# Kernel tuning notes

Measured on AMD Instinct MI355X. Metric: run time of the kernel, lower is better.

## Reference

```python
import jax, jax.numpy as jnp
import numpy as np

D_MODEL = 768
NUM_HEADS = 12
D_K = D_MODEL // NUM_HEADS


def setup_inputs() -> dict:
    key = jax.random.key(0)
    ks = jax.random.split(key, 11)
    B, S, D = 2, 4096, D_MODEL
    s = 1.0 / np.sqrt(D)
    return {
        "query": jax.random.normal(ks[0], (B, S, D), jnp.float32),
        "key": jax.random.normal(ks[1], (B, S, D), jnp.float32),
        "value": jax.random.normal(ks[2], (B, S, D), jnp.float32),
        "Wq": jax.random.normal(ks[3], (D, D), jnp.float32) * s,
        "bq": jnp.zeros((D,), jnp.float32),
        "Wk": jax.random.normal(ks[4], (D, D), jnp.float32) * s,
        "bk": jnp.zeros((D,), jnp.float32),
        "Wv": jax.random.normal(ks[5], (D, D), jnp.float32) * s,
        "bv": jnp.zeros((D,), jnp.float32),
        "Wo": jax.random.normal(ks[6], (D, D), jnp.float32) * s,
        "bo": jnp.zeros((D,), jnp.float32),
    }


def reference(query, key, value, Wq, bq, Wk, bk, Wv, bv, Wo, bo):
    B, S, D = query.shape
    H, dk = NUM_HEADS, D_K
    # torch Linear: y = x @ W^T + b
    def proj(x, W, b):
        return (x @ W.T + b).reshape(B, S, H, dk).transpose(0, 2, 1, 3)  # [B,H,S,dk]
    q = proj(query, Wq, bq)
    k = proj(key, Wk, bk)
    v = proj(value, Wv, bv)
    scores = jnp.einsum("bhqd,bhkd->bhqk", q, k) / jnp.sqrt(jnp.float32(dk))
    attn = jax.nn.softmax(scores, axis=-1)  # dropout is identity in eval mode
    x = jnp.einsum("bhqk,bhkd->bhqd", attn, v)
    x = x.transpose(0, 2, 1, 3).reshape(B, S, D)
    return x @ Wo.T + bo
```

## Files before the change

### kernel.cpp

```cpp
#include <hip/hip_runtime.h>
#include <hip/hip_bf16.h>


typedef __attribute__((ext_vector_type(8))) short short8;
typedef __attribute__((ext_vector_type(4))) float floatx4;
typedef __attribute__((ext_vector_type(4))) float float4v;

#define S_LEN 4096
#define D_MODEL 768
#define NUM_HEADS 12
#define DK 64
#define BATCH 2
#define M_ROWS (BATCH * S_LEN)
#define HEADS_TOTAL (BATCH * NUM_HEADS)
#define QSCALE 0.1803368801111204f

__device__ __forceinline__ unsigned short f2bf(float f) {
    union { float f; unsigned int i; } v; v.f = f;
    unsigned int r = v.i + 0x7fff + ((v.i >> 16) & 1);
    return (unsigned short)(r >> 16);
}

__device__ __forceinline__ unsigned int cvt_pk_bf16(float a, float b) {
    unsigned int r;
    asm("v_cvt_pk_bf16_f32 %0, %1, %2" : "=v"(r) : "v"(a), "v"(b));
    return r;
}

__device__ __forceinline__ float exp2_fast(float x) {
    float r;
    asm("v_exp_f32 %0, %1" : "=v"(r) : "v"(x));
    return r;
}

__device__ __forceinline__ int swz(int r, int c) {
    return (r << 6) + ((((c >> 3) ^ (r & 7)) << 3) | (c & 7));
}

__device__ __forceinline__ void pack8(const float4v& f0, const float4v& f1,
                                      unsigned short* __restrict__ dst) {
    uint4 w;
    w.x = cvt_pk_bf16(f0[0], f0[1]);
    w.y = cvt_pk_bf16(f0[2], f0[3]);
    w.z = cvt_pk_bf16(f1[0], f1[1]);
    w.w = cvt_pk_bf16(f1[2], f1[3]);
    *(uint4*)dst = w;
}

__device__ __forceinline__ void bar_lgkm() {
    asm volatile("s_waitcnt lgkmcnt(0)" ::: "memory");
    __builtin_amdgcn_s_barrier();
    __builtin_amdgcn_sched_barrier(0);
}

template <int MODE, int XF32>
__global__ __launch_bounds__(256, 2) void gemm_bt(
    const void* __restrict__ Xv,
    const float* __restrict__ W,
    const float* __restrict__ bias,
    void* __restrict__ outv,
    int M, int N, int K)
{
    __shared__ __align__(16) unsigned short As[2][8192];
    __shared__ __align__(16) unsigned short Bs[2][6144];

    const int t    = threadIdx.x;
    const int wv   = t >> 6;
    const int lane = t & 63;
    const int l15  = lane & 15;
    const int quad = lane >> 4;
    const int wm   = wv >> 1;
    const int wn   = wv & 1;

    const int bid = blockIdx.x;
    const int wg  = (bid & 7) * 64 + (bid >> 3);
    const int m0  = (wg >> 3) * 128;
    const int n0  = (wg & 7) * 96;

    floatx4 acc[4][3];
#pragma unroll
    for (int i = 0; i < 4; ++i)
#pragma unroll
        for (int j = 0; j < 3; ++j) acc[i][j] = (floatx4){0.f, 0.f, 0.f, 0.f};

    const int sr   = t >> 3;
    const int scol = (t & 7) * 8;
    const int st0  = swz(sr, scol);

    float4v xaE[8], xaO[8];
    uint4   xuE[4], xuO[4];
    float4v waE[6], waO[6];

#define G_LOAD(xa, xu, wa, step)                                                         \
    do {                                                                                 \
        const long kofs = (long)(step) * 64 + scol;                                      \
        _Pragma("unroll")                                                                \
        for (int p = 0; p < 4; ++p) {                                                    \
            if (XF32) {                                                                  \
                const float* xp = (const float*)Xv + (long)(m0 + sr + 32 * p) * K + kofs; \
                xa[2 * p]     = *(const float4v*)xp;                                     \
                xa[2 * p + 1] = *(const float4v*)(xp + 4);                               \
            } else {                                                                     \
                const unsigned short* xp =                                               \
                    (const unsigned short*)Xv + (long)(m0 + sr + 32 * p) * K + kofs;     \
                xu[p] = *(const uint4*)xp;                                               \
            }                                                                            \
        }                                                                                \
        _Pragma("unroll")                                                                \
        for (int p = 0; p < 3; ++p) {                                                    \
            const float* wp = W + (long)(n0 + sr + 32 * p) * K + kofs;                   \
            wa[2 * p]     = *(const float4v*)wp;                                         \
            wa[2 * p + 1] = *(const float4v*)(wp + 4);                                   \
        }                                                                                \
    } while (0)

#define G_WRITE(xa, xu, wa, buf)                                                         \
    do {                                                                                 \
        _Pragma("unroll")                                                                \
        for (int p = 0; p < 4; ++p) {                                                    \
            if (XF32) pack8(xa[2 * p], xa[2 * p + 1], &As[buf][st0 + p * 2048]);         \
            else      *(uint4*)(&As[buf][st0 + p * 2048]) = xu[p];                       \
        }                                                                                \
        _Pragma("unroll")                                                                \
        for (int p = 0; p < 3; ++p)                                                      \
            pack8(wa[2 * p], wa[2 * p + 1], &Bs[buf][st0 + p * 2048]);                   \
    } while (0)

#define DO_MFMA(buf)                                                                     \
    do {                                                                                 \
        const unsigned short* Ab = &As[buf][0];                                          \
        const unsigned short* Bb = &Bs[buf][0];                                          \
        _Pragma("unroll")                                                                \
        for (int kk = 0; kk < 2; ++kk) {                                                 \
            short8 af[4];                                                                \
            _Pragma("unroll")                                                            \
            for (int mi = 0; mi < 4; ++mi)                                               \
                af[mi] = *(const short8*)(Ab + swz(wm * 64 + mi * 16 + l15, kk * 32 + quad * 8)); \
            _Pragma("unroll")                                                            \
            for (int nj = 0; nj < 3; ++nj) {                                             \
                short8 bf = *(const short8*)(Bb + swz(wn * 48 + nj * 16 + l15, kk * 32 + quad * 8)); \
                _Pragma("unroll")                                                        \
                for (int mi = 0; mi < 4; ++mi)                                           \
                    acc[mi][nj] = __builtin_amdgcn_mfma_f32_16x16x32_bf16(af[mi], bf, acc[mi][nj], 0, 0, 0); \
            }                                                                            \
        }                                                                                \
    } while (0)

    const int NS = K / 64;

    G_LOAD(xaE, xuE, waE, 0);
    G_WRITE(xaE, xuE, waE, 0);
    G_LOAD(xaO, xuO, waO, 1);
    __syncthreads();

    for (int s = 0; s < NS - 2; s += 2) {
        DO_MFMA(0);
        G_WRITE(xaO, xuO, waO, 1);
        G_LOAD(xaE, xuE, waE, s + 2);
        bar_lgkm();
        DO_MFMA(1);
        G_WRITE(xaE, xuE, waE, 0);
        if (s + 3 < NS) G_LOAD(xaO, xuO, waO, s + 3);
        bar_lgkm();
    }
    DO_MFMA(0);
    G_WRITE(xaO, xuO, waO, 1);
    bar_lgkm();
    DO_MFMA(1);

#undef G_LOAD
#undef G_WRITE
#undef DO_MFMA

    if (MODE == 2) {
        unsigned short* Sx = &As[0][0];
        __syncthreads();
#pragma unroll
        for (int nj = 0; nj < 3; ++nj) {
            const int colL = wn * 48 + nj * 16 + l15;
            const float bvv = bias[n0 + colL];
#pragma unroll
            for (int mi = 0; mi < 4; ++mi)
#pragma unroll
                for (int reg = 0; reg < 4; ++reg) {
                    const int row = wm * 64 + mi * 16 + quad * 4 + reg;
                    Sx[row * 97 + colL] = f2bf(acc[mi][nj][reg] + bvv);
                }
        }
        __syncthreads();
        const int bb2 = m0 >> 12;
        const int slb = m0 & 4095;
#pragma unroll
        for (int p = 0; p < 6; ++p) {
            const int ci   = t + (p << 8);
            const int colL = ci >> 4;
            const int s8   = (ci & 15) << 3;
            const int dg   = n0 + colL;
            const int h    = dg >> 6;
            const int d    = dg & 63;
            unsigned short w[8];
#pragma unroll
            for (int j = 0; j < 8; ++j) w[j] = Sx[(s8 + j) * 97 + colL];
            unsigned short* outp = (unsigned short*)outv +
                ((long)((bb2 * NUM_HEADS + h) * DK + d)) * S_LEN + slb + s8;
            *(uint4*)outp = *(uint4*)w;
        }
        return;
    }

#pragma unroll
    for (int nj = 0; nj < 3; ++nj) {
        const int col = n0 + wn * 48 + nj * 16 + l15;
        const float bv = bias[col];
#pragma unroll
        for (int mi = 0; mi < 4; ++mi)
#pragma unroll
            for (int reg = 0; reg < 4; ++reg) {
                const int row = m0 + wm * 64 + mi * 16 + quad * 4 + reg;
                const float o = acc[mi][nj][reg] + bv;
                if (MODE == 0) {
                    ((float*)outv)[(long)row * N + col] = o;
                } else {
                    const int bb = row >> 12;
                    const int ss = row & 4095;
                    const int h  = col >> 6;
                    const int d  = col & 63;
                    ((unsigned short*)outv)[(((long)bb * NUM_HEADS + h) * S_LEN + ss) * DK + d] = f2bf(o);
                }
            }
    }
}

__global__ __launch_bounds__(256, 6) void flash_attn_fused(
    const float* __restrict__ Xq,
    const float* __restrict__ Wq,
    const float* __restrict__ bq,
    const unsigned short* __restrict__ Kg,
    const unsigned short* __restrict__ VTg,
    unsigned short* __restrict__ ctx)
{
    __shared__ __align__(16) unsigned short Ks[4096];
    __shared__ __align__(16) unsigned short Vt[4096];
    __shared__ __align__(16) unsigned short Pq[4096];

    const int t    = threadIdx.x;
    const int wv   = t >> 6;
    const int lane = t & 63;
    const int l15  = lane & 15;
    const int quad = lane >> 4;
    const int q0   = blockIdx.x * 64;
    const int bh   = blockIdx.y;
    const int bb   = bh / NUM_HEADS;
    const int h    = bh % NUM_HEADS;
    const long kbase = (long)bh * S_LEN * DK;
    const long vbase = (long)bh * DK * S_LEN;

    const int srow = t >> 3;
    const int scol = (t & 7) * 8;

    const int st_a = swz(srow, scol);
    const int st_b = swz(32 + srow, scol);

    {
        floatx4 qacc[4];
#pragma unroll
        for (int i = 0; i < 4; ++i) qacc[i] = (floatx4){0.f, 0.f, 0.f, 0.f};

        for (int k0 = 0; k0 < D_MODEL; k0 += 64) {
            {
                const float* xp = Xq + ((long)bb * S_LEN + q0 + srow) * D_MODEL + k0 + scol;
                float4v a0 = *(const float4v*)xp, a1 = *(const float4v*)(xp + 4);
                const float* xp2 = xp + (long)32 * D_MODEL;
                float4v a2 = *(const float4v*)xp2, a3 = *(const float4v*)(xp2 + 4);
                const float* wp = Wq + (long)(h * DK + srow) * D_MODEL + k0 + scol;
                float4v b0 = *(const float4v*)wp, b1 = *(const float4v*)(wp + 4);
                const float* wp2 = wp + (long)32 * D_MODEL;
                float4v b2 = *(const float4v*)wp2, b3 = *(const float4v*)(wp2 + 4);
                pack8(a0, a1, &Ks[st_a]); pack8(a2, a3, &Ks[st_b]);
                pack8(b0, b1, &Vt[st_a]); pack8(b2, b3, &Vt[st_b]);
            }
            __syncthreads();
#pragma unroll
            for (int kk = 0; kk < 2; ++kk) {
                short8 a = *(const short8*)(&Ks[swz(wv * 16 + l15, kk * 32 + quad * 8)]);
#pragma unroll
                for (int nj = 0; nj < 4; ++nj) {
                    short8 b = *(const short8*)(&Vt[swz(nj * 16 + l15, kk * 32 + quad * 8)]);
                    qacc[nj] = __builtin_amdgcn_mfma_f32_16x16x32_bf16(a, b, qacc[nj], 0, 0, 0);
                }
            }
            __syncthreads();
        }
#pragma unroll
        for (int nj = 0; nj < 4; ++nj) {
            const float bv = bq[h * DK + nj * 16 + l15];
#pragma unroll
            for (int reg = 0; reg < 4; ++reg) {
                const int row = wv * 16 + quad * 4 + reg;
                Pq[swz(row, nj * 16 + l15)] = f2bf((qacc[nj][reg] + bv) * QSCALE);
            }
        }
    }

    uint4 kr0 = *(const uint4*)(Kg + kbase + (long)srow * DK + scol);
    uint4 kr1 = *(const uint4*)(Kg + kbase + (long)(32 + srow) * DK + scol);
    uint4 vr0 = *(const uint4*)(VTg + vbase + (long)srow * S_LEN + scol);
    uint4 vr1 = *(const uint4*)(VTg + vbase + (long)(32 + srow) * S_LEN + scol);

    asm volatile("s_waitcnt lgkmcnt(0)" ::: "memory");
    short8 qfrag[2];
#pragma unroll
    for (int kk = 0; kk < 2; ++kk)
        qfrag[kk] = *(const short8*)(&Pq[swz(wv * 16 + l15, kk * 32 + quad * 8)]);

    *(uint4*)(&Ks[st_a]) = kr0; *(uint4*)(&Ks[st_b]) = kr1;
    *(uint4*)(&Vt[st_a]) = vr0; *(uint4*)(&Vt[st_b]) = vr1;
    __syncthreads();

    float l_loc = 0.f;
    floatx4 acc[4];
#pragma unroll
    for (int i = 0; i < 4; ++i) acc[i] = (floatx4){0.f, 0.f, 0.f, 0.f};

    const unsigned short* kp = Kg + kbase + (long)64 * DK;
    const unsigned short* vp = VTg + vbase + 64;

    for (int tix = 0; tix < 64; ++tix) {
        if (tix < 63) {
            kr0 = *(const uint4*)(kp + (long)srow * DK + scol);
            kr1 = *(const uint4*)(kp + (long)(32 + srow) * DK + scol);
            vr0 = *(const uint4*)(vp + (long)srow * S_LEN + scol);
            vr1 = *(const uint4*)(vp + (long)(32 + srow) * S_LEN + scol);
            kp += (long)64 * DK;
            vp += 64;
        }

        floatx4 sc[4];
#pragma unroll
        for (int i = 0; i < 4; ++i) sc[i] = (floatx4){0.f, 0.f, 0.f, 0.f};
        __builtin_amdgcn_s_setprio(1);
#pragma unroll
        for (int kk = 0; kk < 2; ++kk) {
#pragma unroll
            for (int nj = 0; nj < 4; ++nj) {
                short8 kf = *(const short8*)(&Ks[swz(nj * 16 + l15, kk * 32 + quad * 8)]);
                sc[nj] = __builtin_amdgcn_mfma_f32_16x16x32_bf16(kf, qfrag[kk], sc[nj], 0, 0, 0);
            }
        }
        __builtin_amdgcn_s_setprio(0);

#pragma unroll
        for (int nj = 0; nj < 4; ++nj) {
            const float e0 = exp2_fast(sc[nj][0]);
            const float e1 = exp2_fast(sc[nj][1]);
            const float e2 = exp2_fast(sc[nj][2]);
            const float e3 = exp2_fast(sc[nj][3]);
            l_loc += (e0 + e1) + (e2 + e3);
            uint2 w;
            w.x = cvt_pk_bf16(e0, e1);
            w.y = cvt_pk_bf16(e2, e3);
            *(uint2*)(&Pq[swz(wv * 16 + l15, nj * 16 + quad * 4)]) = w;
        }
        asm volatile("s_waitcnt lgkmcnt(0)" ::: "memory");

        __builtin_amdgcn_s_setprio(1);
#pragma unroll
        for (int kk = 0; kk < 2; ++kk) {
            short8 a = *(const short8*)(&Pq[swz(wv * 16 + l15, kk * 32 + quad * 8)]);
#pragma unroll
            for (int dj = 0; dj < 4; ++dj) {
                short8 b = *(const short8*)(&Vt[swz(dj * 16 + l15, kk * 32 + quad * 8)]);
                acc[dj] = __builtin_amdgcn_mfma_f32_16x16x32_bf16(a, b, acc[dj], 0, 0, 0);
            }
        }
        __builtin_amdgcn_s_setprio(0);

        __syncthreads();
        if (tix < 63) {
            *(uint4*)(&Ks[st_a]) = kr0; *(uint4*)(&Ks[st_b]) = kr1;
            *(uint4*)(&Vt[st_a]) = vr0; *(uint4*)(&Vt[st_b]) = vr1;
        }
        __syncthreads();
    }

    float l_full = l_loc;
    l_full += __shfl_xor(l_full, 16);
    l_full += __shfl_xor(l_full, 32);
    float l_row[4];
#pragma unroll
    for (int reg = 0; reg < 4; ++reg)
        l_row[reg] = __shfl(l_full, quad * 4 + reg);
#pragma unroll
    for (int dj = 0; dj < 4; ++dj) {
#pragma unroll
        for (int reg = 0; reg < 4; ++reg) {
            const int ss = q0 + wv * 16 + quad * 4 + reg;
            const float v = acc[dj][reg] / l_row[reg];
            ctx[((long)bb * S_LEN + ss) * D_MODEL + h * DK + dj * 16 + l15] = f2bf(v);
        }
    }
}

__global__ void fill_sentinel(float* out, long n, float val) {
    long i = (long)blockIdx.x * blockDim.x + threadIdx.x;
    if (i < n) out[i] = val;
}

extern "C" void kernel_launch(void* const* d_in, const int* in_sizes, int n_in,
                              void* d_out, int out_size, void* d_ws, size_t ws_size,
                              hipStream_t stream)
{
    const float* q_in = (const float*)d_in[0];
    const float* k_in = (const float*)d_in[1];
    const float* v_in = (const float*)d_in[2];
    const float* Wq = (const float*)d_in[3];
    const float* bq = (const float*)d_in[4];
    const float* Wk = (const float*)d_in[5];
    const float* bk = (const float*)d_in[6];
    const float* Wv = (const float*)d_in[7];
    const float* bv = (const float*)d_in[8];
    const float* Wo = (const float*)d_in[9];
    const float* bo = (const float*)d_in[10];

    const long NELEM = (long)M_ROWS * D_MODEL;
    const size_t needed = (size_t)(3 * NELEM) * sizeof(unsigned short);

    if (ws_size < needed) {
        const long n = (long)out_size;
        fill_sentinel<<<(n + 255) / 256, 256, 0, stream>>>((float*)d_out, n,
                                                           (float)(ws_size >> 20));
        return;
    }

    unsigned short* ws  = (unsigned short*)d_ws;
    unsigned short* kp  = ws;
    unsigned short* vtp = ws + NELEM;
    unsigned short* ctx = ws + 2 * NELEM;

    const int GG = (M_ROWS / 128) * (D_MODEL / 96);
    gemm_bt<1, 1><<<GG, 256, 0, stream>>>(k_in, Wk, bk, kp, M_ROWS, D_MODEL, D_MODEL);
    gemm_bt<2, 1><<<GG, 256, 0, stream>>>(v_in, Wv, bv, vtp, M_ROWS, D_MODEL, D_MODEL);

    dim3 agrid(S_LEN / 64, HEADS_TOTAL);
    flash_attn_fused<<<agrid, 256, 0, stream>>>(q_in, Wq, bq, kp, vtp, ctx);

    gemm_bt<0, 0><<<GG, 256, 0, stream>>>(ctx, Wo, bo, d_out, M_ROWS, D_MODEL, D_MODEL);
}
```

Baseline: 381.2 us.

## Process two 64-row query groups per attention block to reuse K/V tiles

Each attention workgroup now handles 128 query rows (two groups of 64) instead of 64, so every K and V tile loaded into shared memory feeds twice the MFMA work. This halves global K/V traffic and per-tile barrier overhead relative to compute. In exchange it doubles accumulator and score registers, grows the P/Q shared buffer, lowers the launch-bounds occupancy hint from 6 to 3, and halves the grid size.

```diff
diff --git a/kernel.cpp b/kernel.cpp
--- a/kernel.cpp
+++ b/kernel.cpp
@@ -231,7 +231,7 @@
     }
 }
 
-__global__ __launch_bounds__(256, 6) void flash_attn_fused(
+__global__ __launch_bounds__(256, 3) void flash_attn_fused(
     const float* __restrict__ Xq,
     const float* __restrict__ Wq,
     const float* __restrict__ bq,
@@ -241,14 +241,14 @@
 {
     __shared__ __align__(16) unsigned short Ks[4096];
     __shared__ __align__(16) unsigned short Vt[4096];
-    __shared__ __align__(16) unsigned short Pq[4096];
+    __shared__ __align__(16) unsigned short Pq[8192];
 
     const int t    = threadIdx.x;
     const int wv   = t >> 6;
     const int lane = t & 63;
     const int l15  = lane & 15;
     const int quad = lane >> 4;
-    const int q0   = blockIdx.x * 64;
+    const int q0   = blockIdx.x * 128;
     const int bh   = blockIdx.y;
     const int bb   = bh / NUM_HEADS;
     const int h    = bh % NUM_HEADS;
@@ -261,14 +261,15 @@
     const int st_a = swz(srow, scol);
     const int st_b = swz(32 + srow, scol);
 
-    {
+#pragma unroll 1
+    for (int g = 0; g < 2; ++g) {
         floatx4 qacc[4];
 #pragma unroll
         for (int i = 0; i < 4; ++i) qacc[i] = (floatx4){0.f, 0.f, 0.f, 0.f};
 
         for (int k0 = 0; k0 < D_MODEL; k0 += 64) {
             {
-                const float* xp = Xq + ((long)bb * S_LEN + q0 + srow) * D_MODEL + k0 + scol;
+                const float* xp = Xq + ((long)bb * S_LEN + q0 + g * 64 + srow) * D_MODEL + k0 + scol;
                 float4v a0 = *(const float4v*)xp, a1 = *(const float4v*)(xp + 4);
                 const float* xp2 = xp + (long)32 * D_MODEL;
                 float4v a2 = *(const float4v*)xp2, a3 = *(const float4v*)(xp2 + 4);
@@ -296,7 +297,7 @@
             const float bv = bq[h * DK + nj * 16 + l15];
 #pragma unroll
             for (int reg = 0; reg < 4; ++reg) {
-                const int row = wv * 16 + quad * 4 + reg;
+                const int row = g * 64 + wv * 16 + quad * 4 + reg;
                 Pq[swz(row, nj * 16 + l15)] = f2bf((qacc[nj][reg] + bv) * QSCALE);
             }
         }
@@ -308,19 +309,23 @@
     uint4 vr1 = *(const uint4*)(VTg + vbase + (long)(32 + srow) * S_LEN + scol);
 
     asm volatile("s_waitcnt lgkmcnt(0)" ::: "memory");
-    short8 qfrag[2];
-#pragma unroll
-    for (int kk = 0; kk < 2; ++kk)
-        qfrag[kk] = *(const short8*)(&Pq[swz(wv * 16 + l15, kk * 32 + quad * 8)]);
+    short8 qfrag[2][2];
+#pragma unroll
+    for (int g = 0; g < 2; ++g)
+#pragma unroll
+        for (int kk = 0; kk < 2; ++kk)
+            qfrag[g][kk] = *(const short8*)(&Pq[swz(g * 64 + wv * 16 + l15, kk * 32 + quad * 8)]);
 
     *(uint4*)(&Ks[st_a]) = kr0; *(uint4*)(&Ks[st_b]) = kr1;
     *(uint4*)(&Vt[st_a]) = vr0; *(uint4*)(&Vt[st_b]) = vr1;
     __syncthreads();
 
-    float l_loc = 0.f;
-    floatx4 acc[4];
-#pragma unroll
-    for (int i = 0; i < 4; ++i) acc[i] = (floatx4){0.f, 0.f, 0.f, 0.f};
+    float l_loc[2] = {0.f, 0.f};
+    floatx4 acc[2][4];
+#pragma unroll
+    for (int g = 0; g < 2; ++g)
+#pragma unroll
+        for (int i = 0; i < 4; ++i) acc[g][i] = (floatx4){0.f, 0.f, 0.f, 0.f};
 
     const unsigned short* kp = Kg + kbase + (long)64 * DK;
     const unsigned short* vp = VTg + vbase + 64;
@@ -335,42 +340,49 @@
             vp += 64;
         }
 
-        floatx4 sc[4];
-#pragma unroll
-        for (int i = 0; i < 4; ++i) sc[i] = (floatx4){0.f, 0.f, 0.f, 0.f};
+        floatx4 sc[2][4];
+#pragma unroll
+        for (int g = 0; g < 2; ++g)
+#pragma unroll
+            for (int i = 0; i < 4; ++i) sc[g][i] = (floatx4){0.f, 0.f, 0.f, 0.f};
         __builtin_amdgcn_s_setprio(1);
 #pragma unroll
         for (int kk = 0; kk < 2; ++kk) {
 #pragma unroll
             for (int nj = 0; nj < 4; ++nj) {
                 short8 kf = *(const short8*)(&Ks[swz(nj * 16 + l15, kk * 32 + quad * 8)]);
-                sc[nj] = __builtin_amdgcn_mfma_f32_16x16x32_bf16(kf, qfrag[kk], sc[nj], 0, 0, 0);
+                sc[0][nj] = __builtin_amdgcn_mfma_f32_16x16x32_bf16(kf, qfrag[0][kk], sc[0][nj], 0, 0, 0);
+                sc[1][nj] = __builtin_amdgcn_mfma_f32_16x16x32_bf16(kf, qfrag[1][kk], sc[1][nj], 0, 0, 0);
             }
         }
         __builtin_amdgcn_s_setprio(0);
 
 #pragma unroll
-        for (int nj = 0; nj < 4; ++nj) {
-            const float e0 = exp2_fast(sc[nj][0]);
-            const float e1 = exp2_fast(sc[nj][1]);
-            const float e2 = exp2_fast(sc[nj][2]);
-            const float e3 = exp2_fast(sc[nj][3]);
-            l_loc += (e0 + e1) + (e2 + e3);
-            uint2 w;
-            w.x = cvt_pk_bf16(e0, e1);
-            w.y = cvt_pk_bf16(e2, e3);
-            *(uint2*)(&Pq[swz(wv * 16 + l15, nj * 16 + quad * 4)]) = w;
-        }
+        for (int g = 0; g < 2; ++g)
+#pragma unroll
+            for (int nj = 0; nj < 4; ++nj) {
+                const float e0 = exp2_fast(sc[g][nj][0]);
+                const float e1 = exp2_fast(sc[g][nj][1]);
+                const float e2 = exp2_fast(sc[g][nj][2]);
+                const float e3 = exp2_fast(sc[g][nj][3]);
+                l_loc[g] += (e0 + e1) + (e2 + e3);
+                uint2 w;
+                w.x = cvt_pk_bf16(e0, e1);
+                w.y = cvt_pk_bf16(e2, e3);
+                *(uint2*)(&Pq[swz(g * 64 + wv * 16 + l15, nj * 16 + quad * 4)]) = w;
+            }
         asm volatile("s_waitcnt lgkmcnt(0)" ::: "memory");
 
         __builtin_amdgcn_s_setprio(1);
 #pragma unroll
         for (int kk = 0; kk < 2; ++kk) {
-            short8 a = *(const short8*)(&Pq[swz(wv * 16 + l15, kk * 32 + quad * 8)]);
+            short8 a0 = *(const short8*)(&Pq[swz(wv * 16 + l15, kk * 32 + quad * 8)]);
+            short8 a1 = *(const short8*)(&Pq[swz(64 + wv * 16 + l15, kk * 32 + quad * 8)]);
 #pragma unroll
             for (int dj = 0; dj < 4; ++dj) {
                 short8 b = *(const short8*)(&Vt[swz(dj * 16 + l15, kk * 32 + quad * 8)]);
-                acc[dj] = __builtin_amdgcn_mfma_f32_16x16x32_bf16(a, b, acc[dj], 0, 0, 0);
+                acc[0][dj] = __builtin_amdgcn_mfma_f32_16x16x32_bf16(a0, b, acc[0][dj], 0, 0, 0);
+                acc[1][dj] = __builtin_amdgcn_mfma_f32_16x16x32_bf16(a1, b, acc[1][dj], 0, 0, 0);
             }
         }
         __builtin_amdgcn_s_setprio(0);
@@ -383,20 +395,23 @@
         __syncthreads();
     }
 
-    float l_full = l_loc;
-    l_full += __shfl_xor(l_full, 16);
-    l_full += __shfl_xor(l_full, 32);
-    float l_row[4];
-#pragma unroll
-    for (int reg = 0; reg < 4; ++reg)
-        l_row[reg] = __shfl(l_full, quad * 4 + reg);
-#pragma unroll
-    for (int dj = 0; dj < 4; ++dj) {
-#pragma unroll
-        for (int reg = 0; reg < 4; ++reg) {
-            const int ss = q0 + wv * 16 + quad * 4 + reg;
-            const float v = acc[dj][reg] / l_row[reg];
-            ctx[((long)bb * S_LEN + ss) * D_MODEL + h * DK + dj * 16 + l15] = f2bf(v);
+#pragma unroll
+    for (int g = 0; g < 2; ++g) {
+        float l_full = l_loc[g];
+        l_full += __shfl_xor(l_full, 16);
+        l_full += __shfl_xor(l_full, 32);
+        float l_row[4];
+#pragma unroll
+        for (int reg = 0; reg < 4; ++reg)
+            l_row[reg] = __shfl(l_full, quad * 4 + reg);
+#pragma unroll
+        for (int dj = 0; dj < 4; ++dj) {
+#pragma unroll
+            for (int reg = 0; reg < 4; ++reg) {
+                const int ss = q0 + g * 64 + wv * 16 + quad * 4 + reg;
+                const float v = acc[g][dj][reg] / l_row[reg];
+                ctx[((long)bb * S_LEN + ss) * D_MODEL + h * DK + dj * 16 + l15] = f2bf(v);
+            }
         }
     }
 }
@@ -441,7 +456,7 @@
     gemm_bt<1, 1><<<GG, 256, 0, stream>>>(k_in, Wk, bk, kp, M_ROWS, D_MODEL, D_MODEL);
     gemm_bt<2, 1><<<GG, 256, 0, stream>>>(v_in, Wv, bv, vtp, M_ROWS, D_MODEL, D_MODEL);
 
-    dim3 agrid(S_LEN / 64, HEADS_TOTAL);
+    dim3 agrid(S_LEN / 128, HEADS_TOTAL);
     flash_attn_fused<<<agrid, 256, 0, stream>>>(q_in, Wq, bq, kp, vtp, ctx);
 
     gemm_bt<0, 0><<<GG, 256, 0, stream>>>(ctx, Wo, bo, d_out, M_ROWS, D_MODEL, D_MODEL);
```

Result: faster. 341.9 us (-10.3%).
